# Kernel optimization log

Measured on AMD Instinct MI355X. Metric: run time of the kernel, lower is better.

The kernel has to match this reference:

```python
import jax, jax.numpy as jnp
import numpy as np

NV, NC, E = 100000, 50000, 800000
VD, CD, H, ROUNDS = 4, 1, 128, 2


def _ln(x, g, b):
    mu = jnp.mean(x, axis=-1, keepdims=True)
    v = jnp.mean((x - mu) ** 2, axis=-1, keepdims=True)
    return (x - mu) * jax.lax.rsqrt(v + 1e-5) * g + b


def _agg(msg, dst, n):
    # degree-normalized scatter-add: out[v] = sum_{e: dst[e]=v} msg[e] / (deg(v)+1e-6)
    s = jax.ops.segment_sum(msg, dst, num_segments=n)
    cnt = jax.ops.segment_sum(jnp.ones((msg.shape[0],), msg.dtype), dst, num_segments=n)
    return s / (cnt[:, None] + 1e-6)


def setup_inputs() -> dict:
    key = jax.random.key(0)
    ks = jax.random.split(key, 16)
    p = lambda k, sh: jax.random.normal(k, sh, jnp.float32) * 0.05
    z = lambda: jnp.zeros((H,), jnp.float32)
    o = lambda: jnp.ones((H,), jnp.float32)
    return {
        'x_var': jax.random.normal(ks[0], (NV, VD), jnp.float32),
        'x_con': jax.random.normal(ks[1], (NC, CD), jnp.float32),
        'e_vc_src': jax.random.randint(ks[2], (E,), 0, NV, jnp.int32),
        'e_vc_dst': jax.random.randint(ks[3], (E,), 0, NC, jnp.int32),
        'e_cv_src': jax.random.randint(ks[4], (E,), 0, NC, jnp.int32),
        'e_cv_dst': jax.random.randint(ks[5], (E,), 0, NV, jnp.int32),
        'var_proj_w': p(ks[6], (VD, H)), 'var_proj_b': z(),
        'con_proj_w': p(ks[7], (CD, H)), 'con_proj_b': z(),
        'v2c_msg_w': p(ks[8], (H, H)), 'v2c_msg_b': z(),
        'v2c_upd_w': p(ks[9], (H + 1, H)), 'v2c_upd_b': z(),
        'v2c_ln_g': o(), 'v2c_ln_b': z(),
        'c2v_msg_w': p(ks[10], (H, H)), 'c2v_msg_b': z(),
        'c2v_ln_g': o(), 'c2v_ln_b': z(),
        'var_gate_w': p(ks[11], (2 * H, H)), 'var_gate_b': z(),
        'con_gate_w': p(ks[12], (2 * H, H)), 'con_gate_b': z(),
        'var_ln_g': o(), 'var_ln_b': z(),
        'con_ln_g': o(), 'con_ln_b': z(),
    }


def reference(x_var, x_con, e_vc_src, e_vc_dst, e_cv_src, e_cv_dst,
              var_proj_w, var_proj_b, con_proj_w, con_proj_b,
              v2c_msg_w, v2c_msg_b, v2c_upd_w, v2c_upd_b, v2c_ln_g, v2c_ln_b,
              c2v_msg_w, c2v_msg_b, c2v_ln_g, c2v_ln_b,
              var_gate_w, var_gate_b, con_gate_w, con_gate_b,
              var_ln_g, var_ln_b, con_ln_g, con_ln_b):
    clue = x_con[:, 0]  # (NC,)
    hv = _ln(jax.nn.relu(x_var @ var_proj_w + var_proj_b), var_ln_g, var_ln_b)  # (NV,H)
    hc = _ln(jax.nn.relu(x_con @ con_proj_w + con_proj_b), con_ln_g, con_ln_b)  # (NC,H)
    for _ in range(ROUNDS):
        # var -> con
        msg = hv[e_vc_src] @ v2c_msg_w + v2c_msg_b  # (E,H)
        agg = _agg(msg, e_vc_dst, NC)
        upd = jnp.concatenate([agg, clue[:, None]], axis=1)  # (NC,H+1)
        con_new = _ln(jax.nn.relu(upd @ v2c_upd_w + v2c_upd_b), v2c_ln_g, v2c_ln_b)
        g = jax.nn.sigmoid(jnp.concatenate([hc, con_new], axis=1) @ con_gate_w + con_gate_b)
        hc = g * con_new + (1 - g) * hc
        # con -> var
        msg2 = hc[e_cv_src] @ c2v_msg_w + c2v_msg_b  # (E,H)
        var_new = _ln(jax.nn.relu(_agg(msg2, e_cv_dst, NV)), c2v_ln_g, c2v_ln_b)
        g2 = jax.nn.sigmoid(jnp.concatenate([hv, var_new], axis=1) @ var_gate_w + var_gate_b)
        hv = g2 * var_new + (1 - g2) * hv
    return hv
```

## Files before the change

### kernel.cpp

```cpp
#include <hip/hip_runtime.h>
#include <stdint.h>

#define NVN 100000
#define NCN 50000
#define NE  800000
#define H   128

typedef __attribute__((ext_vector_type(8))) short bf16x8;
typedef __attribute__((ext_vector_type(4))) float f32x4;

static __device__ __forceinline__ float wredsum(float v) {
#pragma unroll
  for (int off = 32; off > 0; off >>= 1) v += __shfl_xor(v, off, 64);
  return v;
}
static __device__ __forceinline__ float sigmoidf(float x) { return 1.0f / (1.0f + __expf(-x)); }
static __device__ __forceinline__ unsigned short f2bf(float f) {
  unsigned int u = __float_as_uint(f);
  return (unsigned short)((u + 0x7FFFu + ((u >> 16) & 1u)) >> 16);
}
static __device__ __forceinline__ short2 splitbf(float f) {
  unsigned short h = f2bf(f);
  float hf = __uint_as_float(((unsigned int)h) << 16);
  short2 r;
  r.x = (short)h;
  r.y = (short)f2bf(f - hf);
  return r;
}

__global__ __launch_bounds__(256) void k_init_var(const float* __restrict__ xv,
    const float* __restrict__ w, const float* __restrict__ b,
    const float* __restrict__ g, const float* __restrict__ bb,
    float* __restrict__ hv, unsigned short* __restrict__ hb) {
  int wid = (blockIdx.x * 256 + threadIdx.x) >> 6;
  int lane = threadIdx.x & 63;
  if (wid >= NVN) return;
  float x0 = xv[wid*4+0], x1 = xv[wid*4+1], x2 = xv[wid*4+2], x3 = xv[wid*4+3];
  int c0 = lane, c1 = lane + 64;
  float v0 = b[c0] + x0*w[c0] + x1*w[H+c0] + x2*w[2*H+c0] + x3*w[3*H+c0];
  float v1 = b[c1] + x0*w[c1] + x1*w[H+c1] + x2*w[2*H+c1] + x3*w[3*H+c1];
  v0 = fmaxf(v0, 0.f); v1 = fmaxf(v1, 0.f);
  float mu = wredsum(v0 + v1) * (1.0f/H);
  float d0 = v0 - mu, d1 = v1 - mu;
  float var = wredsum(d0*d0 + d1*d1) * (1.0f/H);
  float r = rsqrtf(var + 1e-5f);
  float o0 = d0*r*g[c0] + bb[c0], o1 = d1*r*g[c1] + bb[c1];
  hv[(size_t)wid*H + c0] = o0;  hv[(size_t)wid*H + c1] = o1;
  hb[(size_t)wid*H + c0] = f2bf(o0);  hb[(size_t)wid*H + c1] = f2bf(o1);
}

__global__ __launch_bounds__(256) void k_init_con(const float* __restrict__ xc,
    const float* __restrict__ w, const float* __restrict__ b,
    const float* __restrict__ g, const float* __restrict__ bb,
    float* __restrict__ hc, unsigned short* __restrict__ hb) {
  int wid = (blockIdx.x * 256 + threadIdx.x) >> 6;
  int lane = threadIdx.x & 63;
  if (wid >= NCN) return;
  float x = xc[wid];
  int c0 = lane, c1 = lane + 64;
  float v0 = fmaxf(b[c0] + x*w[c0], 0.f);
  float v1 = fmaxf(b[c1] + x*w[c1], 0.f);
  float mu = wredsum(v0 + v1) * (1.0f/H);
  float d0 = v0 - mu, d1 = v1 - mu;
  float var = wredsum(d0*d0 + d1*d1) * (1.0f/H);
  float r = rsqrtf(var + 1e-5f);
  float o0 = d0*r*g[c0] + bb[c0], o1 = d1*r*g[c1] + bb[c1];
  hc[(size_t)wid*H + c0] = o0;  hc[(size_t)wid*H + c1] = o1;
  hb[(size_t)wid*H + c0] = f2bf(o0);  hb[(size_t)wid*H + c1] = f2bf(o1);
}

__global__ void k_fuse_w(const float* __restrict__ wm, const float* __restrict__ wu,
                         float* __restrict__ wf) {
  int idx = blockIdx.x*256 + threadIdx.x;
  int i = idx >> 7, j = idx & 127;
  float a = 0.f;
  for (int k = 0; k < H; ++k) a = fmaf(wm[i*H+k], wu[k*H+j], a);
  wf[idx] = a;
}
__global__ void k_fuse_b(const float* __restrict__ bm, const float* __restrict__ wu,
                         float* __restrict__ bf) {
  int j = threadIdx.x;
  float a = 0.f;
  for (int k = 0; k < H; ++k) a = fmaf(bm[k], wu[k*H+j], a);
  bf[j] = a;
}

__global__ __launch_bounds__(256) void k_perm2(const float* __restrict__ W,
    unsigned short* __restrict__ Whi, unsigned short* __restrict__ Wlo, int K) {
  int idx = blockIdx.x*256 + threadIdx.x;
  if (idx >= K*H) return;
  int j = idx & 7, lane = (idx >> 3) & 63, ct = (idx >> 9) & 7, kb = idx >> 12;
  int k = kb*32 + (lane >> 4)*8 + j, c = ct*16 + (lane & 15);
  float w = W[k*H + c];
  unsigned short h = f2bf(w);
  float hf = __uint_as_float(((unsigned int)h) << 16);
  Whi[idx] = h;
  Wlo[idx] = f2bf(w - hf);
}

__global__ void k_count(const int* __restrict__ dc, const int* __restrict__ dv,
                        int* __restrict__ cnt_c, int* __restrict__ cnt_v) {
  for (int e = blockIdx.x*blockDim.x + threadIdx.x; e < NE; e += gridDim.x*blockDim.x) {
    atomicAdd(&cnt_c[dc[e]], 1);
    atomicAdd(&cnt_v[dv[e]], 1);
  }
}
__global__ __launch_bounds__(256) void k_scan1(const int* __restrict__ in, int* __restrict__ out,
                                               int* __restrict__ aux, int n) {
  __shared__ int s[256];
  int t = threadIdx.x, i = blockIdx.x*256 + t;
  int v = (i < n) ? in[i] : 0;
  s[t] = v; __syncthreads();
  for (int off = 1; off < 256; off <<= 1) {
    int x = (t >= off) ? s[t - off] : 0;
    __syncthreads();
    s[t] += x;
    __syncthreads();
  }
  if (i < n) out[i] = s[t] - v;
  if (t == 255) aux[blockIdx.x] = s[255];
}
__global__ __launch_bounds__(1024) void k_scan2(int* __restrict__ aux, int nb) {
  __shared__ int s[1024];
  int t = threadIdx.x;
  int v = (t < nb) ? aux[t] : 0;
  s[t] = v; __syncthreads();
  for (int off = 1; off < 1024; off <<= 1) {
    int x = (t >= off) ? s[t-off] : 0;
    __syncthreads();
    s[t] += x;
    __syncthreads();
  }
  if (t < nb) aux[t] = s[t] - v;
}
__global__ __launch_bounds__(256) void k_scan3(int* __restrict__ out, const int* __restrict__ aux,
                                               int n, int total) {
  int i = blockIdx.x*256 + threadIdx.x;
  if (i < n) out[i] += aux[blockIdx.x];
  if (i == 0) out[n] = total;
}
__global__ void k_scatter(const int* __restrict__ sc, const int* __restrict__ dc,
                          const int* __restrict__ sv, const int* __restrict__ dv,
                          const int* __restrict__ off_c, int* __restrict__ cur_c, int* __restrict__ lst_c,
                          const int* __restrict__ off_v, int* __restrict__ cur_v, int* __restrict__ lst_v) {
  for (int e = blockIdx.x*blockDim.x + threadIdx.x; e < NE; e += gridDim.x*blockDim.x) {
    int d = dc[e]; int p = atomicAdd(&cur_c[d], 1); lst_c[off_c[d] + p] = sc[e];
    d = dv[e];     p = atomicAdd(&cur_v[d], 1);     lst_v[off_v[d] + p] = sv[e];
  }
}

__global__ __launch_bounds__(256) void k_gather_bf(const unsigned int* __restrict__ tab,
    const int* __restrict__ off, const int* __restrict__ lst,
    float* __restrict__ out, int n) {
  int wid = (blockIdx.x * 256 + threadIdx.x) >> 6;
  int lane = threadIdx.x & 63;
  if (wid >= n) return;
  int s0 = off[wid], s1 = off[wid+1];
  float a0 = 0.f, a1 = 0.f;
  int p = s0;
  for (; p + 4 <= s1; p += 4) {
    int i0 = lst[p], i1 = lst[p+1], i2 = lst[p+2], i3 = lst[p+3];
    unsigned int u0 = tab[(size_t)i0 * 64 + lane];
    unsigned int u1 = tab[(size_t)i1 * 64 + lane];
    unsigned int u2 = tab[(size_t)i2 * 64 + lane];
    unsigned int u3 = tab[(size_t)i3 * 64 + lane];
    a0 += __uint_as_float(u0 << 16) + __uint_as_float(u1 << 16)
        + __uint_as_float(u2 << 16) + __uint_as_float(u3 << 16);
    a1 += __uint_as_float(u0 & 0xFFFF0000u) + __uint_as_float(u1 & 0xFFFF0000u)
        + __uint_as_float(u2 & 0xFFFF0000u) + __uint_as_float(u3 & 0xFFFF0000u);
  }
  for (; p < s1; ++p) {
    unsigned int u = tab[(size_t)lst[p] * 64 + lane];
    a0 += __uint_as_float(u << 16);
    a1 += __uint_as_float(u & 0xFFFF0000u);
  }
  float inv = 1.0f / ((float)(s1 - s0) + 1e-6f);
  ((float2*)(out + (size_t)wid*H))[lane] = make_float2(a0*inv, a1*inv);
}

template<int EPI>
__global__ __launch_bounds__(256) void k_mle(
    const float* __restrict__ A,
    const unsigned short* __restrict__ Wph, const unsigned short* __restrict__ Wpl,
    const int* __restrict__ cnt, const float* __restrict__ xc,
    const float* __restrict__ vb, const float* __restrict__ wcl,
    const float* __restrict__ badd, const float* __restrict__ lng,
    const float* __restrict__ lnb, float* __restrict__ out, int n) {
  __shared__ float lds[64][132];
  const int wv = threadIdx.x >> 6, lane = threadIdx.x & 63;
  const int rbase = blockIdx.x*64 + wv*16;
  if (rbase >= n) return;
  const int g = lane >> 4, c15 = lane & 15;
  int arow = rbase + c15; if (arow > n-1) arow = n-1;
  const float* Ar = A + (size_t)arow*H + g*8;
  bf16x8 ahi[4], alo[4];
#pragma unroll
  for (int kb = 0; kb < 4; ++kb) {
    float4 p0 = *(const float4*)(Ar + kb*32);
    float4 p1 = *(const float4*)(Ar + kb*32 + 4);
    bf16x8 h, l;
    short2 s;
    s = splitbf(p0.x); h[0] = s.x; l[0] = s.y;
    s = splitbf(p0.y); h[1] = s.x; l[1] = s.y;
    s = splitbf(p0.z); h[2] = s.x; l[2] = s.y;
    s = splitbf(p0.w); h[3] = s.x; l[3] = s.y;
    s = splitbf(p1.x); h[4] = s.x; l[4] = s.y;
    s = splitbf(p1.y); h[5] = s.x; l[5] = s.y;
    s = splitbf(p1.z); h[6] = s.x; l[6] = s.y;
    s = splitbf(p1.w); h[7] = s.x; l[7] = s.y;
    ahi[kb] = h; alo[kb] = l;
  }
  const bf16x8* Bph = (const bf16x8*)Wph;
  const bf16x8* Bpl = (const bf16x8*)Wpl;
  f32x4 zero = {0.f, 0.f, 0.f, 0.f};
  f32x4 acc[8];
#pragma unroll
  for (int ct = 0; ct < 8; ++ct) acc[ct] = zero;
#pragma unroll
  for (int kb = 0; kb < 4; ++kb)
#pragma unroll
    for (int ct = 0; ct < 8; ++ct) {
      bf16x8 bh = Bph[(kb*8+ct)*64 + lane];
      bf16x8 bl = Bpl[(kb*8+ct)*64 + lane];
      acc[ct] = __builtin_amdgcn_mfma_f32_16x16x32_bf16(ahi[kb], bh, acc[ct], 0, 0, 0);
      acc[ct] = __builtin_amdgcn_mfma_f32_16x16x32_bf16(alo[kb], bh, acc[ct], 0, 0, 0);
      acc[ct] = __builtin_amdgcn_mfma_f32_16x16x32_bf16(ahi[kb], bl, acc[ct], 0, 0, 0);
    }
#pragma unroll
  for (int r = 0; r < 4; ++r)
#pragma unroll
    for (int ct = 0; ct < 8; ++ct)
      lds[wv*16 + g*4 + r][ct*16 + c15] = acc[ct][r];
  float vb0 = vb[lane], vb1 = vb[lane+64];
  float lg0 = lng[lane], lg1 = lng[lane+64];
  float lb0 = lnb[lane], lb1 = lnb[lane+64];
  float wc0 = 0.f, wc1 = 0.f, ba0 = 0.f, ba1 = 0.f;
  if constexpr (EPI == 0) {
    wc0 = wcl[lane]; wc1 = wcl[lane+64];
    ba0 = badd[lane]; ba1 = badd[lane+64];
  }
  for (int i = 0; i < 16; ++i) {
    int row = wv*16 + i;
    int dst = blockIdx.x*64 + row;
    if (dst >= n) break;
    float cf = (float)cnt[dst];
    float scale = cf / (cf + 1e-6f);
    float v0 = lds[row][lane]     + scale*vb0;
    float v1 = lds[row][lane+64]  + scale*vb1;
    if constexpr (EPI == 0) {
      float clue = xc[dst];
      v0 += clue*wc0 + ba0;
      v1 += clue*wc1 + ba1;
    }
    v0 = fmaxf(v0, 0.f); v1 = fmaxf(v1, 0.f);
    float mu = wredsum(v0 + v1) * (1.0f/H);
    float d0 = v0 - mu, d1 = v1 - mu;
    float var = wredsum(d0*d0 + d1*d1) * (1.0f/H);
    float r = rsqrtf(var + 1e-5f);
    out[(size_t)dst*H + lane]      = d0*r*lg0 + lb0;
    out[(size_t)dst*H + lane + 64] = d1*r*lg1 + lb1;
  }
}

__global__ __launch_bounds__(256) void k_mm2g(const float* __restrict__ A1,
    const float* __restrict__ A2,
    const unsigned short* __restrict__ Wph,
    const float* __restrict__ gb,
    float* __restrict__ Hm, unsigned short* __restrict__ Hb, int n) {
  const int wv = threadIdx.x >> 6, lane = threadIdx.x & 63;
  const int rbase = blockIdx.x*64 + wv*16;
  if (rbase >= n) return;
  const int g = lane >> 4, c15 = lane & 15;
  int arow = rbase + c15; if (arow > n-1) arow = n-1;
  const float* Ar1 = A1 + (size_t)arow*H + g*8;
  const float* Ar2 = A2 + (size_t)arow*H + g*8;
  bf16x8 ahi[8], alo[8];
#pragma unroll
  for (int kb = 0; kb < 8; ++kb) {
    const float* src = (kb < 4) ? (Ar1 + kb*32) : (Ar2 + (kb-4)*32);
    float4 p0 = *(const float4*)(src);
    float4 p1 = *(const float4*)(src + 4);
    bf16x8 h, l;
    short2 s;
    s = splitbf(p0.x); h[0] = s.x; l[0] = s.y;
    s = splitbf(p0.y); h[1] = s.x; l[1] = s.y;
    s = splitbf(p0.z); h[2] = s.x; l[2] = s.y;
    s = splitbf(p0.w); h[3] = s.x; l[3] = s.y;
    s = splitbf(p1.x); h[4] = s.x; l[4] = s.y;
    s = splitbf(p1.y); h[5] = s.x; l[5] = s.y;
    s = splitbf(p1.z); h[6] = s.x; l[6] = s.y;
    s = splitbf(p1.w); h[7] = s.x; l[7] = s.y;
    ahi[kb] = h; alo[kb] = l;
  }
  const bf16x8* Bph = (const bf16x8*)Wph;
  f32x4 zero = {0.f, 0.f, 0.f, 0.f};
  f32x4 acc[8];
#pragma unroll
  for (int ct = 0; ct < 8; ++ct) acc[ct] = zero;
#pragma unroll
  for (int kb = 0; kb < 8; ++kb)
#pragma unroll
    for (int ct = 0; ct < 8; ++ct) {
      bf16x8 bh = Bph[(kb*8+ct)*64 + lane];
      acc[ct] = __builtin_amdgcn_mfma_f32_16x16x32_bf16(ahi[kb], bh, acc[ct], 0, 0, 0);
      acc[ct] = __builtin_amdgcn_mfma_f32_16x16x32_bf16(alo[kb], bh, acc[ct], 0, 0, 0);
    }
  float gbv[8];
#pragma unroll
  for (int ct = 0; ct < 8; ++ct) gbv[ct] = gb[ct*16 + c15];
#pragma unroll
  for (int r = 0; r < 4; ++r) {
    int rg = rbase + g*4 + r;
    if (rg >= n) continue;
    const float* np = A2 + (size_t)rg*H + c15;
    float* hp = Hm + (size_t)rg*H + c15;
    unsigned short* hbp = Hb + (size_t)rg*H + c15;
#pragma unroll
    for (int ct = 0; ct < 8; ++ct) {
      float gg = sigmoidf(acc[ct][r] + gbv[ct]);
      float nv = np[ct*16], ov = hp[ct*16];
      float res = gg*nv + (1.f - gg)*ov;
      hp[ct*16] = res;
      hbp[ct*16] = f2bf(res);
    }
  }
}

extern "C" void kernel_launch(void* const* d_in, const int* in_sizes, int n_in,
                              void* d_out, int out_size, void* d_ws, size_t ws_size,
                              hipStream_t stream) {
  const float* x_var   = (const float*)d_in[0];
  const float* x_con   = (const float*)d_in[1];
  const int*   evc_src = (const int*)d_in[2];
  const int*   evc_dst = (const int*)d_in[3];
  const int*   ecv_src = (const int*)d_in[4];
  const int*   ecv_dst = (const int*)d_in[5];
  const float* vproj_w = (const float*)d_in[6];
  const float* vproj_b = (const float*)d_in[7];
  const float* cproj_w = (const float*)d_in[8];
  const float* cproj_b = (const float*)d_in[9];
  const float* wmsg    = (const float*)d_in[10];
  const float* bmsg    = (const float*)d_in[11];
  const float* wupd    = (const float*)d_in[12];
  const float* bupd    = (const float*)d_in[13];
  const float* v2c_ln_g = (const float*)d_in[14];
  const float* v2c_ln_b = (const float*)d_in[15];
  const float* wc2v    = (const float*)d_in[16];
  const float* bc2v    = (const float*)d_in[17];
  const float* c2v_ln_g = (const float*)d_in[18];
  const float* c2v_ln_b = (const float*)d_in[19];
  const float* vgate_w = (const float*)d_in[20];
  const float* vgate_b = (const float*)d_in[21];
  const float* cgate_w = (const float*)d_in[22];
  const float* cgate_b = (const float*)d_in[23];
  const float* var_ln_g = (const float*)d_in[24];
  const float* var_ln_b = (const float*)d_in[25];
  const float* con_ln_g = (const float*)d_in[26];
  const float* con_ln_b = (const float*)d_in[27];
  float* hv = (float*)d_out;

  char* p = (char*)d_ws;
  auto carve = [&](size_t bytes) { char* r = p; p += (bytes + 255) & ~(size_t)255; return r; };
  int* cnt_c = (int*)carve((size_t)NCN*4);
  int* cur_c = (int*)carve((size_t)NCN*4);
  int* cnt_v = (int*)carve((size_t)NVN*4);
  int* cur_v = (int*)carve((size_t)NVN*4);
  int* off_c = (int*)carve((size_t)(NCN+1)*4);
  int* off_v = (int*)carve((size_t)(NVN+1)*4);
  int* aux   = (int*)carve(1024*4);
  int* lst_c = (int*)carve((size_t)NE*4);
  int* lst_v = (int*)carve((size_t)NE*4);
  float* wf  = (float*)carve((size_t)H*H*4);
  float* bfu = (float*)carve((size_t)H*4);
  unsigned short* wfph = (unsigned short*)carve((size_t)H*H*2);
  unsigned short* wfpl = (unsigned short*)carve((size_t)H*H*2);
  unsigned short* wvph = (unsigned short*)carve((size_t)H*H*2);
  unsigned short* wvpl = (unsigned short*)carve((size_t)H*H*2);
  unsigned short* cgph = (unsigned short*)carve((size_t)2*H*H*2);
  unsigned short* cgpl = (unsigned short*)carve((size_t)2*H*H*2);
  unsigned short* vgph = (unsigned short*)carve((size_t)2*H*H*2);
  unsigned short* vgpl = (unsigned short*)carve((size_t)2*H*H*2);
  float* hc    = (float*)carve((size_t)NCN*H*4);
  float* c_new = (float*)carve((size_t)NCN*H*4);
  float* v_new = (float*)carve((size_t)NVN*H*4);
  float* t_c   = (float*)carve((size_t)NCN*H*4);
  float* t_v   = (float*)carve((size_t)NVN*H*4);
  unsigned short* hvb = (unsigned short*)carve((size_t)NVN*H*2);
  unsigned short* hcb = (unsigned short*)carve((size_t)NCN*H*2);
  if ((size_t)(p - (char*)d_ws) > ws_size) return;

  (void)hipMemsetAsync(cnt_c, 0, (size_t)NCN*4, stream);
  (void)hipMemsetAsync(cur_c, 0, (size_t)NCN*4, stream);
  (void)hipMemsetAsync(cnt_v, 0, (size_t)NVN*4, stream);
  (void)hipMemsetAsync(cur_v, 0, (size_t)NVN*4, stream);

  k_fuse_w<<<64, 256, 0, stream>>>(wmsg, wupd, wf);
  k_fuse_b<<<1, 128, 0, stream>>>(bmsg, wupd, bfu);
  k_perm2<<<(H*H+255)/256, 256, 0, stream>>>(wf, wfph, wfpl, H);
  k_perm2<<<(H*H+255)/256, 256, 0, stream>>>(wc2v, wvph, wvpl, H);
  k_perm2<<<(2*H*H+255)/256, 256, 0, stream>>>(cgate_w, cgph, cgpl, 2*H);
  k_perm2<<<(2*H*H+255)/256, 256, 0, stream>>>(vgate_w, vgph, vgpl, 2*H);

  k_count<<<1024, 256, 0, stream>>>(evc_dst, ecv_dst, cnt_c, cnt_v);
  int nbc = (NCN + 255)/256, nbv = (NVN + 255)/256;
  k_scan1<<<nbc, 256, 0, stream>>>(cnt_c, off_c, aux, NCN);
  k_scan2<<<1, 1024, 0, stream>>>(aux, nbc);
  k_scan3<<<nbc, 256, 0, stream>>>(off_c, aux, NCN, NE);
  k_scan1<<<nbv, 256, 0, stream>>>(cnt_v, off_v, aux, NVN);
  k_scan2<<<1, 1024, 0, stream>>>(aux, nbv);
  k_scan3<<<nbv, 256, 0, stream>>>(off_v, aux, NVN, NE);
  k_scatter<<<1024, 256, 0, stream>>>(evc_src, evc_dst, ecv_src, ecv_dst,
                                      off_c, cur_c, lst_c, off_v, cur_v, lst_v);

  k_init_var<<<NVN/4, 256, 0, stream>>>(x_var, vproj_w, vproj_b, var_ln_g, var_ln_b, hv, hvb);
  k_init_con<<<NCN/4, 256, 0, stream>>>(x_con, cproj_w, cproj_b, con_ln_g, con_ln_b, hc, hcb);

  for (int r = 0; r < 2; ++r) {
    k_gather_bf<<<(NCN+3)/4, 256, 0, stream>>>((const unsigned int*)hvb, off_c, lst_c, t_c, NCN);
    k_mle<0><<<(NCN+63)/64, 256, 0, stream>>>(t_c, wfph, wfpl, cnt_c, x_con, bfu, wupd + H*H,
                                              bupd, v2c_ln_g, v2c_ln_b, c_new, NCN);
    k_mm2g<<<(NCN+63)/64, 256, 0, stream>>>(hc, c_new, cgph, cgate_b, hc, hcb, NCN);
    k_gather_bf<<<(NVN+3)/4, 256, 0, stream>>>((const unsigned int*)hcb, off_v, lst_v, t_v, NVN);
    k_mle<1><<<(NVN+63)/64, 256, 0, stream>>>(t_v, wvph, wvpl, cnt_v, nullptr, bc2v, nullptr,
                                              nullptr, c2v_ln_g, c2v_ln_b, v_new, NVN);
    k_mm2g<<<(NVN+63)/64, 256, 0, stream>>>(hv, v_new, vgph, vgate_b, hv, hvb, NVN);
  }
}
```

Measured before the change: 727.9 us.

## Fuse update-MLP/LayerNorm kernel with gated residual GEMM via LDS

Merges the message-update GEMM plus LayerNorm kernel with the following gate GEMM and blend kernel. The normalized new state now stays in shared memory and feeds the gate matmul's second input, instead of being written to and re-read from global buffers. This removes one launch per half-round and the global round trip of the c_new and v_new intermediates. In exchange the fused kernel holds more registers and has more serial phases per block, which may lower occupancy.

```diff
diff --git a/kernel.cpp b/kernel.cpp
--- a/kernel.cpp
+++ b/kernel.cpp
@@ -179,149 +179,149 @@
 }
 
 template<int EPI>
-__global__ __launch_bounds__(256) void k_mle(
+__global__ __launch_bounds__(256) void k_mleg(
     const float* __restrict__ A,
     const unsigned short* __restrict__ Wph, const unsigned short* __restrict__ Wpl,
     const int* __restrict__ cnt, const float* __restrict__ xc,
     const float* __restrict__ vb, const float* __restrict__ wcl,
     const float* __restrict__ badd, const float* __restrict__ lng,
-    const float* __restrict__ lnb, float* __restrict__ out, int n) {
+    const float* __restrict__ lnb,
+    const unsigned short* __restrict__ Gph, const float* __restrict__ gb,
+    float* __restrict__ Hm, unsigned short* __restrict__ Hb, int n) {
   __shared__ float lds[64][132];
   const int wv = threadIdx.x >> 6, lane = threadIdx.x & 63;
   const int rbase = blockIdx.x*64 + wv*16;
   if (rbase >= n) return;
   const int g = lane >> 4, c15 = lane & 15;
   int arow = rbase + c15; if (arow > n-1) arow = n-1;
-  const float* Ar = A + (size_t)arow*H + g*8;
-  bf16x8 ahi[4], alo[4];
-#pragma unroll
-  for (int kb = 0; kb < 4; ++kb) {
-    float4 p0 = *(const float4*)(Ar + kb*32);
-    float4 p1 = *(const float4*)(Ar + kb*32 + 4);
-    bf16x8 h, l;
-    short2 s;
-    s = splitbf(p0.x); h[0] = s.x; l[0] = s.y;
-    s = splitbf(p0.y); h[1] = s.x; l[1] = s.y;
-    s = splitbf(p0.z); h[2] = s.x; l[2] = s.y;
-    s = splitbf(p0.w); h[3] = s.x; l[3] = s.y;
-    s = splitbf(p1.x); h[4] = s.x; l[4] = s.y;
-    s = splitbf(p1.y); h[5] = s.x; l[5] = s.y;
-    s = splitbf(p1.z); h[6] = s.x; l[6] = s.y;
-    s = splitbf(p1.w); h[7] = s.x; l[7] = s.y;
-    ahi[kb] = h; alo[kb] = l;
-  }
-  const bf16x8* Bph = (const bf16x8*)Wph;
-  const bf16x8* Bpl = (const bf16x8*)Wpl;
-  f32x4 zero = {0.f, 0.f, 0.f, 0.f};
-  f32x4 acc[8];
-#pragma unroll
-  for (int ct = 0; ct < 8; ++ct) acc[ct] = zero;
-#pragma unroll
-  for (int kb = 0; kb < 4; ++kb)
-#pragma unroll
-    for (int ct = 0; ct < 8; ++ct) {
-      bf16x8 bh = Bph[(kb*8+ct)*64 + lane];
-      bf16x8 bl = Bpl[(kb*8+ct)*64 + lane];
-      acc[ct] = __builtin_amdgcn_mfma_f32_16x16x32_bf16(ahi[kb], bh, acc[ct], 0, 0, 0);
-      acc[ct] = __builtin_amdgcn_mfma_f32_16x16x32_bf16(alo[kb], bh, acc[ct], 0, 0, 0);
-      acc[ct] = __builtin_amdgcn_mfma_f32_16x16x32_bf16(ahi[kb], bl, acc[ct], 0, 0, 0);
+
+  {
+    const float* Ar = A + (size_t)arow*H + g*8;
+    bf16x8 ahi[4], alo[4];
+#pragma unroll
+    for (int kb = 0; kb < 4; ++kb) {
+      float4 p0 = *(const float4*)(Ar + kb*32);
+      float4 p1 = *(const float4*)(Ar + kb*32 + 4);
+      bf16x8 h, l;
+      short2 s;
+      s = splitbf(p0.x); h[0] = s.x; l[0] = s.y;
+      s = splitbf(p0.y); h[1] = s.x; l[1] = s.y;
+      s = splitbf(p0.z); h[2] = s.x; l[2] = s.y;
+      s = splitbf(p0.w); h[3] = s.x; l[3] = s.y;
+      s = splitbf(p1.x); h[4] = s.x; l[4] = s.y;
+      s = splitbf(p1.y); h[5] = s.x; l[5] = s.y;
+      s = splitbf(p1.z); h[6] = s.x; l[6] = s.y;
+      s = splitbf(p1.w); h[7] = s.x; l[7] = s.y;
+      ahi[kb] = h; alo[kb] = l;
     }
-#pragma unroll
-  for (int r = 0; r < 4; ++r)
-#pragma unroll
-    for (int ct = 0; ct < 8; ++ct)
-      lds[wv*16 + g*4 + r][ct*16 + c15] = acc[ct][r];
-  float vb0 = vb[lane], vb1 = vb[lane+64];
-  float lg0 = lng[lane], lg1 = lng[lane+64];
-  float lb0 = lnb[lane], lb1 = lnb[lane+64];
-  float wc0 = 0.f, wc1 = 0.f, ba0 = 0.f, ba1 = 0.f;
-  if constexpr (EPI == 0) {
-    wc0 = wcl[lane]; wc1 = wcl[lane+64];
-    ba0 = badd[lane]; ba1 = badd[lane+64];
-  }
-  for (int i = 0; i < 16; ++i) {
-    int row = wv*16 + i;
-    int dst = blockIdx.x*64 + row;
-    if (dst >= n) break;
-    float cf = (float)cnt[dst];
-    float scale = cf / (cf + 1e-6f);
-    float v0 = lds[row][lane]     + scale*vb0;
-    float v1 = lds[row][lane+64]  + scale*vb1;
+    const bf16x8* Bph = (const bf16x8*)Wph;
+    const bf16x8* Bpl = (const bf16x8*)Wpl;
+    f32x4 zero = {0.f, 0.f, 0.f, 0.f};
+    f32x4 acc[8];
+#pragma unroll
+    for (int ct = 0; ct < 8; ++ct) acc[ct] = zero;
+#pragma unroll
+    for (int kb = 0; kb < 4; ++kb)
+#pragma unroll
+      for (int ct = 0; ct < 8; ++ct) {
+        bf16x8 bh = Bph[(kb*8+ct)*64 + lane];
+        bf16x8 bl = Bpl[(kb*8+ct)*64 + lane];
+        acc[ct] = __builtin_amdgcn_mfma_f32_16x16x32_bf16(ahi[kb], bh, acc[ct], 0, 0, 0);
+        acc[ct] = __builtin_amdgcn_mfma_f32_16x16x32_bf16(alo[kb], bh, acc[ct], 0, 0, 0);
+        acc[ct] = __builtin_amdgcn_mfma_f32_16x16x32_bf16(ahi[kb], bl, acc[ct], 0, 0, 0);
+      }
+#pragma unroll
+    for (int r = 0; r < 4; ++r)
+#pragma unroll
+      for (int ct = 0; ct < 8; ++ct)
+        lds[wv*16 + g*4 + r][ct*16 + c15] = acc[ct][r];
+  }
+
+  {
+    float vb0 = vb[lane], vb1 = vb[lane+64];
+    float lg0 = lng[lane], lg1 = lng[lane+64];
+    float lb0 = lnb[lane], lb1 = lnb[lane+64];
+    float wc0 = 0.f, wc1 = 0.f, ba0 = 0.f, ba1 = 0.f;
     if constexpr (EPI == 0) {
-      float clue = xc[dst];
-      v0 += clue*wc0 + ba0;
-      v1 += clue*wc1 + ba1;
+      wc0 = wcl[lane]; wc1 = wcl[lane+64];
+      ba0 = badd[lane]; ba1 = badd[lane+64];
     }
-    v0 = fmaxf(v0, 0.f); v1 = fmaxf(v1, 0.f);
-    float mu = wredsum(v0 + v1) * (1.0f/H);
-    float d0 = v0 - mu, d1 = v1 - mu;
-    float var = wredsum(d0*d0 + d1*d1) * (1.0f/H);
-    float r = rsqrtf(var + 1e-5f);
-    out[(size_t)dst*H + lane]      = d0*r*lg0 + lb0;
-    out[(size_t)dst*H + lane + 64] = d1*r*lg1 + lb1;
-  }
-}
-
-__global__ __launch_bounds__(256) void k_mm2g(const float* __restrict__ A1,
-    const float* __restrict__ A2,
-    const unsigned short* __restrict__ Wph,
-    const float* __restrict__ gb,
-    float* __restrict__ Hm, unsigned short* __restrict__ Hb, int n) {
-  const int wv = threadIdx.x >> 6, lane = threadIdx.x & 63;
-  const int rbase = blockIdx.x*64 + wv*16;
-  if (rbase >= n) return;
-  const int g = lane >> 4, c15 = lane & 15;
-  int arow = rbase + c15; if (arow > n-1) arow = n-1;
-  const float* Ar1 = A1 + (size_t)arow*H + g*8;
-  const float* Ar2 = A2 + (size_t)arow*H + g*8;
-  bf16x8 ahi[8], alo[8];
-#pragma unroll
-  for (int kb = 0; kb < 8; ++kb) {
-    const float* src = (kb < 4) ? (Ar1 + kb*32) : (Ar2 + (kb-4)*32);
-    float4 p0 = *(const float4*)(src);
-    float4 p1 = *(const float4*)(src + 4);
-    bf16x8 h, l;
-    short2 s;
-    s = splitbf(p0.x); h[0] = s.x; l[0] = s.y;
-    s = splitbf(p0.y); h[1] = s.x; l[1] = s.y;
-    s = splitbf(p0.z); h[2] = s.x; l[2] = s.y;
-    s = splitbf(p0.w); h[3] = s.x; l[3] = s.y;
-    s = splitbf(p1.x); h[4] = s.x; l[4] = s.y;
-    s = splitbf(p1.y); h[5] = s.x; l[5] = s.y;
-    s = splitbf(p1.z); h[6] = s.x; l[6] = s.y;
-    s = splitbf(p1.w); h[7] = s.x; l[7] = s.y;
-    ahi[kb] = h; alo[kb] = l;
-  }
-  const bf16x8* Bph = (const bf16x8*)Wph;
-  f32x4 zero = {0.f, 0.f, 0.f, 0.f};
-  f32x4 acc[8];
-#pragma unroll
-  for (int ct = 0; ct < 8; ++ct) acc[ct] = zero;
-#pragma unroll
-  for (int kb = 0; kb < 8; ++kb)
-#pragma unroll
-    for (int ct = 0; ct < 8; ++ct) {
-      bf16x8 bh = Bph[(kb*8+ct)*64 + lane];
-      acc[ct] = __builtin_amdgcn_mfma_f32_16x16x32_bf16(ahi[kb], bh, acc[ct], 0, 0, 0);
-      acc[ct] = __builtin_amdgcn_mfma_f32_16x16x32_bf16(alo[kb], bh, acc[ct], 0, 0, 0);
+    for (int i = 0; i < 16; ++i) {
+      int row = wv*16 + i;
+      int dst = blockIdx.x*64 + row;
+      if (dst >= n) break;
+      float cf = (float)cnt[dst];
+      float scale = cf / (cf + 1e-6f);
+      float v0 = lds[row][lane]     + scale*vb0;
+      float v1 = lds[row][lane+64]  + scale*vb1;
+      if constexpr (EPI == 0) {
+        float clue = xc[dst];
+        v0 += clue*wc0 + ba0;
+        v1 += clue*wc1 + ba1;
+      }
+      v0 = fmaxf(v0, 0.f); v1 = fmaxf(v1, 0.f);
+      float mu = wredsum(v0 + v1) * (1.0f/H);
+      float d0 = v0 - mu, d1 = v1 - mu;
+      float var = wredsum(d0*d0 + d1*d1) * (1.0f/H);
+      float r = rsqrtf(var + 1e-5f);
+      lds[row][lane]      = d0*r*lg0 + lb0;
+      lds[row][lane + 64] = d1*r*lg1 + lb1;
     }
-  float gbv[8];
-#pragma unroll
-  for (int ct = 0; ct < 8; ++ct) gbv[ct] = gb[ct*16 + c15];
-#pragma unroll
-  for (int r = 0; r < 4; ++r) {
-    int rg = rbase + g*4 + r;
-    if (rg >= n) continue;
-    const float* np = A2 + (size_t)rg*H + c15;
-    float* hp = Hm + (size_t)rg*H + c15;
-    unsigned short* hbp = Hb + (size_t)rg*H + c15;
-#pragma unroll
-    for (int ct = 0; ct < 8; ++ct) {
-      float gg = sigmoidf(acc[ct][r] + gbv[ct]);
-      float nv = np[ct*16], ov = hp[ct*16];
-      float res = gg*nv + (1.f - gg)*ov;
-      hp[ct*16] = res;
-      hbp[ct*16] = f2bf(res);
+  }
+
+  {
+    bf16x8 ahi[8], alo[8];
+    const float* Ar1 = Hm + (size_t)arow*H + g*8;
+    const float* Ar2 = &lds[wv*16 + c15][g*8];
+#pragma unroll
+    for (int kb = 0; kb < 8; ++kb) {
+      const float* src = (kb < 4) ? (Ar1 + kb*32) : (Ar2 + (kb-4)*32);
+      float4 p0 = *(const float4*)(src);
+      float4 p1 = *(const float4*)(src + 4);
+      bf16x8 h, l;
+      short2 s;
+      s = splitbf(p0.x); h[0] = s.x; l[0] = s.y;
+      s = splitbf(p0.y); h[1] = s.x; l[1] = s.y;
+      s = splitbf(p0.z); h[2] = s.x; l[2] = s.y;
+      s = splitbf(p0.w); h[3] = s.x; l[3] = s.y;
+      s = splitbf(p1.x); h[4] = s.x; l[4] = s.y;
+      s = splitbf(p1.y); h[5] = s.x; l[5] = s.y;
+      s = splitbf(p1.z); h[6] = s.x; l[6] = s.y;
+      s = splitbf(p1.w); h[7] = s.x; l[7] = s.y;
+      ahi[kb] = h; alo[kb] = l;
+    }
+    const bf16x8* Bph = (const bf16x8*)Gph;
+    f32x4 zero = {0.f, 0.f, 0.f, 0.f};
+    f32x4 acc[8];
+#pragma unroll
+    for (int ct = 0; ct < 8; ++ct) acc[ct] = zero;
+#pragma unroll
+    for (int kb = 0; kb < 8; ++kb)
+#pragma unroll
+      for (int ct = 0; ct < 8; ++ct) {
+        bf16x8 bh = Bph[(kb*8+ct)*64 + lane];
+        acc[ct] = __builtin_amdgcn_mfma_f32_16x16x32_bf16(ahi[kb], bh, acc[ct], 0, 0, 0);
+        acc[ct] = __builtin_amdgcn_mfma_f32_16x16x32_bf16(alo[kb], bh, acc[ct], 0, 0, 0);
+      }
+    float gbv[8];
+#pragma unroll
+    for (int ct = 0; ct < 8; ++ct) gbv[ct] = gb[ct*16 + c15];
+#pragma unroll
+    for (int r = 0; r < 4; ++r) {
+      int rg = rbase + g*4 + r;
+      if (rg >= n) continue;
+      int row = wv*16 + g*4 + r;
+      float* hp = Hm + (size_t)rg*H + c15;
+      unsigned short* hbp = Hb + (size_t)rg*H + c15;
+#pragma unroll
+      for (int ct = 0; ct < 8; ++ct) {
+        float gg = sigmoidf(acc[ct][r] + gbv[ct]);
+        float nv = lds[row][ct*16 + c15];
+        float ov = hp[ct*16];
+        float res = gg*nv + (1.f - gg)*ov;
+        hp[ct*16] = res;
+        hbp[ct*16] = f2bf(res);
+      }
     }
   }
 }
@@ -381,8 +381,6 @@
   unsigned short* vgph = (unsigned short*)carve((size_t)2*H*H*2);
   unsigned short* vgpl = (unsigned short*)carve((size_t)2*H*H*2);
   float* hc    = (float*)carve((size_t)NCN*H*4);
-  float* c_new = (float*)carve((size_t)NCN*H*4);
-  float* v_new = (float*)carve((size_t)NVN*H*4);
   float* t_c   = (float*)carve((size_t)NCN*H*4);
   float* t_v   = (float*)carve((size_t)NVN*H*4);
   unsigned short* hvb = (unsigned short*)carve((size_t)NVN*H*2);
@@ -417,12 +415,12 @@
 
   for (int r = 0; r < 2; ++r) {
     k_gather_bf<<<(NCN+3)/4, 256, 0, stream>>>((const unsigned int*)hvb, off_c, lst_c, t_c, NCN);
-    k_mle<0><<<(NCN+63)/64, 256, 0, stream>>>(t_c, wfph, wfpl, cnt_c, x_con, bfu, wupd + H*H,
-                                              bupd, v2c_ln_g, v2c_ln_b, c_new, NCN);
-    k_mm2g<<<(NCN+63)/64, 256, 0, stream>>>(hc, c_new, cgph, cgate_b, hc, hcb, NCN);
+    k_mleg<0><<<(NCN+63)/64, 256, 0, stream>>>(t_c, wfph, wfpl, cnt_c, x_con, bfu, wupd + H*H,
+                                               bupd, v2c_ln_g, v2c_ln_b, cgph, cgate_b,
+                                               hc, hcb, NCN);
     k_gather_bf<<<(NVN+3)/4, 256, 0, stream>>>((const unsigned int*)hcb, off_v, lst_v, t_v, NVN);
-    k_mle<1><<<(NVN+63)/64, 256, 0, stream>>>(t_v, wvph, wvpl, cnt_v, nullptr, bc2v, nullptr,
-                                              nullptr, c2v_ln_g, c2v_ln_b, v_new, NVN);
-    k_mm2g<<<(NVN+63)/64, 256, 0, stream>>>(hv, v_new, vgph, vgate_b, hv, hvb, NVN);
-  }
-}
+    k_mleg<1><<<(NVN+63)/64, 256, 0, stream>>>(t_v, wvph, wvpl, cnt_v, nullptr, bc2v, nullptr,
+                                               nullptr, c2v_ln_g, c2v_ln_b, vgph, vgate_b,
+                                               hv, hvb, NVN);
+  }
+}
```

Result: faster. 661.9 us (-9.1%).
